# Kernel tuning notes

Measured on AMD Instinct MI355X. Metric: run time of the kernel, lower is better.

## Reference

```python
import jax, jax.numpy as jnp
import numpy as np

B, S, D, H = 4, 2048, 1024, 16
HD = D // H

def setup_inputs() -> dict:
    key = jax.random.key(0)
    ks = jax.random.split(key, 5)
    scale = 1.0 / np.sqrt(D)
    x = jax.random.normal(ks[0], (B, S, D), dtype=jnp.float32)
    w_qkv = jax.random.normal(ks[1], (D, 3 * D), dtype=jnp.float32) * scale
    b_qkv = jax.random.normal(ks[2], (3 * D,), dtype=jnp.float32) * 0.01
    w_proj = jax.random.normal(ks[3], (D, D), dtype=jnp.float32) * scale
    b_proj = jax.random.normal(ks[4], (D,), dtype=jnp.float32) * 0.01
    return {"x": x, "w_qkv": w_qkv, "b_qkv": b_qkv, "w_proj": w_proj, "b_proj": b_proj}

def reference(x, w_qkv, b_qkv, w_proj, b_proj):
    b, s, d = x.shape
    qkv = x @ w_qkv + b_qkv                      # [B,S,3D]
    qkv = qkv.reshape(b, s, 3, H, HD)
    q, k, v = jnp.moveaxis(qkv, 2, 0)            # each [B,S,H,HD]
    q = q.transpose(0, 2, 1, 3)                  # [B,H,S,HD]
    k = k.transpose(0, 2, 1, 3)
    v = v.transpose(0, 2, 1, 3)
    scale = 1.0 / jnp.sqrt(jnp.asarray(HD, dtype=x.dtype))
    scores = jnp.einsum('bhqd,bhkd->bhqk', q, k) * scale
    attn = jax.nn.softmax(scores, axis=-1)
    out = jnp.einsum('bhqk,bhkd->bhqd', attn, v)  # [B,H,S,HD]
    out = out.transpose(0, 2, 1, 3).reshape(b, s, d)
    return out @ w_proj + b_proj
```

## Files before the change

kernel.cpp:

```cpp
#include <hip/hip_runtime.h>

#define B_  4
#define S_  2048
#define D_  1024
#define H_  16
#define HD_ 64
#define M_  (B_*S_)
#define QSCALE 0.1803368801111204f

typedef unsigned short u16;
typedef __bf16 bf16x8 __attribute__((ext_vector_type(8)));
typedef __bf16 bf16x2 __attribute__((ext_vector_type(2)));
typedef float  f32x4  __attribute__((ext_vector_type(4)));
typedef float  f32x16 __attribute__((ext_vector_type(16)));

__device__ __forceinline__ u16 f2bf(float f) {
  unsigned int u = __float_as_uint(f);
  u += 0x7fffu + ((u >> 16) & 1u);
  return (u16)(u >> 16);
}
__device__ __forceinline__ unsigned int packbf2(float lo, float hi) {
#if __has_builtin(__builtin_amdgcn_cvt_pk_bf16_f32)
  union { bf16x2 v; unsigned int u; } c;
  c.v = __builtin_amdgcn_cvt_pk_bf16_f32(lo, hi);
  return c.u;
#else
  return (unsigned int)f2bf(lo) | ((unsigned int)f2bf(hi) << 16);
#endif
}
__device__ __forceinline__ void gld16(const void* g, void* l) {
  __builtin_amdgcn_global_load_lds(
      (const __attribute__((address_space(1))) unsigned int*)g,
      (__attribute__((address_space(3))) unsigned int*)l, 16, 0, 0);
}
#define MFMA32(a,b,c) __builtin_amdgcn_mfma_f32_32x32x16_bf16(a,b,c,0,0,0)
#define MFMA16(a,b,c) __builtin_amdgcn_mfma_f32_16x16x32_bf16(a,b,c,0,0,0)

__global__ void cvt_f32_bf16(const float* __restrict__ in, u16* __restrict__ out, int n4) {
  int i = blockIdx.x * 256 + threadIdx.x;
  if (i < n4) {
    float4 v = ((const float4*)in)[i];
    ((uint2*)out)[i] = make_uint2(packbf2(v.x, v.y), packbf2(v.z, v.w));
  }
}

__global__ void transpose_w(const float* __restrict__ in, u16* __restrict__ out, int R, int C) {
  __shared__ float tile[32][33];
  int c0 = blockIdx.x * 32, r0 = blockIdx.y * 32;
  int tx = threadIdx.x, ty = threadIdx.y;
  #pragma unroll
  for (int i = 0; i < 4; i++)
    tile[ty + i*8][tx] = in[(size_t)(r0 + ty + i*8) * C + c0 + tx];
  __syncthreads();
  #pragma unroll
  for (int i = 0; i < 4; i++)
    out[(size_t)(c0 + ty + i*8) * R + r0 + tx] = f2bf(tile[tx][ty + i*8]);
}

__global__ void transpose_v(const u16* __restrict__ in, u16* __restrict__ out) {
  __shared__ u16 tile[32][33];
  size_t base = (size_t)blockIdx.z * S_ * HD_;
  int c0 = blockIdx.x * 32, r0 = blockIdx.y * 32;
  int tx = threadIdx.x, ty = threadIdx.y;
  #pragma unroll
  for (int i = 0; i < 4; i++)
    tile[ty + i*8][tx] = in[base + (size_t)(r0 + ty + i*8) * HD_ + c0 + tx];
  __syncthreads();
  #pragma unroll
  for (int i = 0; i < 4; i++)
    out[base + (size_t)(c0 + ty + i*8) * S_ + r0 + tx] = tile[tx][ty + i*8];
}

__global__ __launch_bounds__(256) void gemm_qkv(
    const u16* __restrict__ X, const u16* __restrict__ WT,
    const float* __restrict__ bias,
    u16* __restrict__ qb, u16* __restrict__ kb, u16* __restrict__ vb)
{
  __shared__ u16 Al[128 * 40];
  __shared__ u16 Bl[128 * 40];
  const int t = threadIdx.x;
  const int m0 = blockIdx.y * 128;
  const int n0 = blockIdx.x * 128;
  const int wave = t >> 6, lane = t & 63;
  const int wm = (wave >> 1) * 64, wn = (wave & 1) * 64;
  const int lr = lane & 15, quad = lane >> 4;

  f32x4 acc[4][4] = {};
  for (int k0 = 0; k0 < D_; k0 += 32) {
    __syncthreads();
    #pragma unroll
    for (int i = 0; i < 2; i++) {
      int c = t + i * 256;
      int row = c >> 2, ko = (c & 3) * 8;
      *(uint4*)&Al[row * 40 + ko] = *(const uint4*)&X [(size_t)(m0 + row) * D_ + k0 + ko];
      *(uint4*)&Bl[row * 40 + ko] = *(const uint4*)&WT[(size_t)(n0 + row) * D_ + k0 + ko];
    }
    __syncthreads();
    bf16x8 a[4], b[4];
    #pragma unroll
    for (int mt = 0; mt < 4; mt++) a[mt] = *(const bf16x8*)&Al[(wm + mt*16 + lr) * 40 + quad * 8];
    #pragma unroll
    for (int nt = 0; nt < 4; nt++) b[nt] = *(const bf16x8*)&Bl[(wn + nt*16 + lr) * 40 + quad * 8];
    #pragma unroll
    for (int mt = 0; mt < 4; mt++)
      #pragma unroll
      for (int nt = 0; nt < 4; nt++)
        acc[mt][nt] = MFMA16(a[mt], b[nt], acc[mt][nt]);
  }
  #pragma unroll
  for (int mt = 0; mt < 4; mt++)
  #pragma unroll
  for (int nt = 0; nt < 4; nt++)
  #pragma unroll
  for (int r = 0; r < 4; r++) {
    int m = m0 + wm + mt * 16 + quad * 4 + r;
    int n = n0 + wn + nt * 16 + lr;
    float v = acc[mt][nt][r] + bias[n];
    int which = n >> 10;
    int h = (n >> 6) & 15, hd = n & 63;
    int bb = m >> 11, s = m & 2047;
    size_t idx = (((size_t)(bb * H_ + h) * S_) + s) * HD_ + hd;
    if (which == 0)      qb[idx] = f2bf(v * QSCALE);
    else if (which == 1) kb[idx] = f2bf(v);
    else                 vb[idx] = f2bf(v);
  }
}

__global__ __launch_bounds__(256) void gemm_proj(
    const u16* __restrict__ X, const u16* __restrict__ WT,
    const float* __restrict__ bias, float* __restrict__ out)
{
  __shared__ u16 Al[128 * 40];
  __shared__ u16 Bl[128 * 40];
  const int t = threadIdx.x;
  const int m0 = blockIdx.y * 128;
  const int n0 = blockIdx.x * 128;
  const int wave = t >> 6, lane = t & 63;
  const int wm = (wave >> 1) * 64, wn = (wave & 1) * 64;
  const int lr = lane & 15, quad = lane >> 4;

  f32x4 acc[4][4] = {};
  for (int k0 = 0; k0 < D_; k0 += 32) {
    __syncthreads();
    #pragma unroll
    for (int i = 0; i < 2; i++) {
      int c = t + i * 256;
      int row = c >> 2, ko = (c & 3) * 8;
      *(uint4*)&Al[row * 40 + ko] = *(const uint4*)&X [(size_t)(m0 + row) * D_ + k0 + ko];
      *(uint4*)&Bl[row * 40 + ko] = *(const uint4*)&WT[(size_t)(n0 + row) * D_ + k0 + ko];
    }
    __syncthreads();
    bf16x8 a[4], b[4];
    #pragma unroll
    for (int mt = 0; mt < 4; mt++) a[mt] = *(const bf16x8*)&Al[(wm + mt*16 + lr) * 40 + quad * 8];
    #pragma unroll
    for (int nt = 0; nt < 4; nt++) b[nt] = *(const bf16x8*)&Bl[(wn + nt*16 + lr) * 40 + quad * 8];
    #pragma unroll
    for (int mt = 0; mt < 4; mt++)
      #pragma unroll
      for (int nt = 0; nt < 4; nt++)
        acc[mt][nt] = MFMA16(a[mt], b[nt], acc[mt][nt]);
  }
  #pragma unroll
  for (int mt = 0; mt < 4; mt++)
  #pragma unroll
  for (int nt = 0; nt < 4; nt++)
  #pragma unroll
  for (int r = 0; r < 4; r++) {
    int m = m0 + wm + mt * 16 + quad * 4 + r;
    int n = n0 + wn + nt * 16 + lr;
    out[(size_t)m * D_ + n] = acc[mt][nt][r] + bias[n];
  }
}

__global__ __launch_bounds__(128,2) void attn(
    const u16* __restrict__ qb, const u16* __restrict__ kb,
    const u16* __restrict__ vt, u16* __restrict__ ob)
{
  __shared__ u16 Kl[8*512];
  __shared__ u16 Vl[8*512];
  __shared__ float redL[2][64];
  const int t = threadIdx.x, w = t >> 6, l = t & 63, l31 = l & 31, h = l >> 5;
  const int bh = blockIdx.y, b = bh >> 4, hh = bh & 15;
  const int s0 = blockIdx.x * 128 + w * 64;
  const u16* qp = qb + (size_t)bh * S_ * HD_;
  const u16* kp = kb + (size_t)bh * S_ * HD_;
  const u16* vp = vt + (size_t)bh * HD_ * S_;

  bf16x8 qa[2][4];
  #pragma unroll
  for (int g = 0; g < 2; g++)
    #pragma unroll
    for (int kk = 0; kk < 4; kk++)
      qa[g][kk] = *(const bf16x8*)(qp + (size_t)(s0 + g*32 + l31)*HD_ + kk*16 + h*8);

  f32x16 o[2][2] = {};
  float l_[2] = {0.f, 0.f};

  for (int k0 = 0; k0 < S_; k0 += 64) {
    __syncthreads();
    #pragma unroll
    for (int j = 0; j < 4; j++) {
      gld16(kp + (size_t)(k0 + w*32 + l31)*HD_ + j*16 + h*8, (char*)Kl + (w*4+j)*1024);
      gld16(vp + (size_t)(w*32 + l31)*S_ + k0 + j*16 + h*8, (char*)Vl + (w*4+j)*1024);
    }
    __syncthreads();

    f32x16 sf[2][2] = {};
    #pragma unroll
    for (int kk = 0; kk < 4; kk++) {
      bf16x8 ka0 = *(const bf16x8*)(Kl + (0*4+kk)*512 + l*8);
      bf16x8 ka1 = *(const bf16x8*)(Kl + (1*4+kk)*512 + l*8);
      sf[0][0] = MFMA32(ka0, qa[0][kk], sf[0][0]);
      sf[0][1] = MFMA32(ka0, qa[1][kk], sf[0][1]);
      sf[1][0] = MFMA32(ka1, qa[0][kk], sf[1][0]);
      sf[1][1] = MFMA32(ka1, qa[1][kk], sf[1][1]);
    }

    unsigned int pk[2][2][4][2];
    #pragma unroll
    for (int g = 0; g < 2; g++) {
      float sa = 0.f, sb = 0.f, sc = 0.f, sd = 0.f;
      #pragma unroll
      for (int mt = 0; mt < 2; mt++)
        #pragma unroll
        for (int e = 0; e < 4; e++) {
          float p0 = __builtin_amdgcn_exp2f(sf[mt][g][4*e+0]);
          float p1 = __builtin_amdgcn_exp2f(sf[mt][g][4*e+1]);
          float p2 = __builtin_amdgcn_exp2f(sf[mt][g][4*e+2]);
          float p3 = __builtin_amdgcn_exp2f(sf[mt][g][4*e+3]);
          sa += p0; sb += p1; sc += p2; sd += p3;
          pk[mt][g][e][0] = packbf2(p0, p1);
          pk[mt][g][e][1] = packbf2(p2, p3);
        }
      float s = (sa + sb) + (sc + sd);
      s += __shfl_xor(s, 32);
      l_[g] += s;
    }

    #pragma unroll
    for (int kk2 = 0; kk2 < 4; kk2++) {
      const int mt = kk2 >> 1, k1 = kk2 & 1;
      bf16x8 bv0 = *(const bf16x8*)(Vl + (0*4+kk2)*512 + l*8);
      bf16x8 bv1 = *(const bf16x8*)(Vl + (1*4+kk2)*512 + l*8);
      #pragma unroll
      for (int g = 0; g < 2; g++) {
        unsigned int s0_ = h ? pk[mt][g][2*k1][0] : pk[mt][g][2*k1+1][0];
        unsigned int s1_ = h ? pk[mt][g][2*k1][1] : pk[mt][g][2*k1+1][1];
        unsigned int r0 = (unsigned int)__shfl_xor((int)s0_, 32);
        unsigned int r1 = (unsigned int)__shfl_xor((int)s1_, 32);
        union { unsigned int u[4]; bf16x8 v; } pa;
        pa.u[0] = h ? r0 : pk[mt][g][2*k1][0];
        pa.u[1] = h ? r1 : pk[mt][g][2*k1][1];
        pa.u[2] = h ? pk[mt][g][2*k1+1][0] : r0;
        pa.u[3] = h ? pk[mt][g][2*k1+1][1] : r1;
        o[g][0] = MFMA32(pa.v, bv0, o[g][0]);
        o[g][1] = MFMA32(pa.v, bv1, o[g][1]);
      }
    }
  }

  #pragma unroll
  for (int g = 0; g < 2; g++) redL[w][g*32 + l31] = 1.f / l_[g];
  __syncthreads();
  #pragma unroll
  for (int g = 0; g < 2; g++)
    #pragma unroll
    for (int rb = 0; rb < 4; rb++) {
      f32x4 iv4 = *(const f32x4*)&redL[w][g*32 + 8*rb + 4*h];
      #pragma unroll
      for (int c = 0; c < 4; c++) {
        int r = rb*4 + c;
        int row = s0 + g*32 + c + 8*rb + 4*h;
        size_t off = ((size_t)(b*S_ + row)) * D_ + hh*64;
        ob[off + 0*32 + l31] = f2bf(o[g][0][r] * iv4[c]);
        ob[off + 1*32 + l31] = f2bf(o[g][1][r] * iv4[c]);
      }
    }
}

extern "C" void kernel_launch(void* const* d_in, const int* in_sizes, int n_in,
                              void* d_out, int out_size, void* d_ws, size_t ws_size,
                              hipStream_t stream) {
  const float* x      = (const float*)d_in[0];
  const float* w_qkv  = (const float*)d_in[1];
  const float* b_qkv  = (const float*)d_in[2];
  const float* w_proj = (const float*)d_in[3];
  const float* b_proj = (const float*)d_in[4];
  float* out = (float*)d_out;

  char* ws = (char*)d_ws;
  u16* xbf    = (u16*)ws; ws += (size_t)M_ * D_ * 2;
  u16* wqkvT  = (u16*)ws; ws += (size_t)3 * D_ * D_ * 2;
  u16* wprojT = (u16*)ws; ws += (size_t)D_ * D_ * 2;
  u16* qbuf   = (u16*)ws; ws += (size_t)M_ * D_ * 2;
  u16* kbuf   = (u16*)ws; ws += (size_t)M_ * D_ * 2;
  u16* vbuf   = (u16*)ws; ws += (size_t)M_ * D_ * 2;
  u16* vtbuf  = (u16*)ws; ws += (size_t)M_ * D_ * 2;
  u16* aobuf  = (u16*)ws; ws += (size_t)M_ * D_ * 2;

  cvt_f32_bf16<<<(M_ * D_ / 4 + 255) / 256, 256, 0, stream>>>(x, xbf, M_ * D_ / 4);
  transpose_w<<<dim3(3 * D_ / 32, D_ / 32), dim3(32, 8), 0, stream>>>(w_qkv, wqkvT, D_, 3 * D_);
  transpose_w<<<dim3(D_ / 32, D_ / 32), dim3(32, 8), 0, stream>>>(w_proj, wprojT, D_, D_);
  gemm_qkv<<<dim3(3 * D_ / 128, M_ / 128), 256, 0, stream>>>(xbf, wqkvT, b_qkv, qbuf, kbuf, vbuf);
  transpose_v<<<dim3(HD_ / 32, S_ / 32, B_ * H_), dim3(32, 8), 0, stream>>>(vbuf, vtbuf);
  attn<<<dim3(S_ / 128, B_ * H_), 128, 0, stream>>>(qbuf, kbuf, vtbuf, aobuf);
  gemm_proj<<<dim3(D_ / 128, M_ / 128), 256, 0, stream>>>(aobuf, wprojT, b_proj, out);
}
```

Baseline: 324.2 us.

## Pre-tile operands into MFMA fragment layout and double-buffer LDS with async loads

Producer kernels now write X, the weights, Q/K, V and the attention output directly in a tiled layout that matches the MFMA fragment order. The GEMM and attention kernels can then use contiguous global_load_lds copies into double-buffered shared memory, prefetching the next tile while computing the current one. The separate V transpose kernel and its buffer are removed because the QKV GEMM epilogue writes V already transposed. The producers now do scattered 2-byte stores, and the larger LDS footprint may limit occupancy.

```diff
diff --git a/kernel.cpp b/kernel.cpp
--- a/kernel.cpp
+++ b/kernel.cpp
@@ -36,11 +36,27 @@
 #define MFMA32(a,b,c) __builtin_amdgcn_mfma_f32_32x32x16_bf16(a,b,c,0,0,0)
 #define MFMA16(a,b,c) __builtin_amdgcn_mfma_f32_16x16x32_bf16(a,b,c,0,0,0)
 
+__device__ __forceinline__ size_t off16e(int r, int k) {
+  return ((size_t)((r >> 7) * 32 + (k >> 5))) * 4096
+       + (size_t)((r >> 4) & 7) * 512
+       + (size_t)(((k >> 3) & 3) * 16 + (r & 15)) * 8 + (k & 7);
+}
+__device__ __forceinline__ size_t offA32(int bh, int s, int hd) {
+  return ((size_t)(bh * 32 + (s >> 6)) * 8 + ((s >> 5) & 1) * 4 + (hd >> 4)) * 512
+       + (size_t)(((hd >> 3) & 1) * 32 + (s & 31)) * 8 + (hd & 7);
+}
+__device__ __forceinline__ size_t offVT(int bh, int s, int hd) {
+  return ((size_t)(bh * 32 + (s >> 6)) * 8 + (hd >> 5) * 4 + ((s >> 4) & 3)) * 512
+       + (size_t)(((s >> 3) & 1) * 32 + (hd & 31)) * 8 + (s & 7);
+}
+
 __global__ void cvt_f32_bf16(const float* __restrict__ in, u16* __restrict__ out, int n4) {
   int i = blockIdx.x * 256 + threadIdx.x;
   if (i < n4) {
     float4 v = ((const float4*)in)[i];
-    ((uint2*)out)[i] = make_uint2(packbf2(v.x, v.y), packbf2(v.z, v.w));
+    int m = i >> 8;
+    int k = (i & 255) * 4;
+    *(uint2*)&out[off16e(m, k)] = make_uint2(packbf2(v.x, v.y), packbf2(v.z, v.w));
   }
 }
 
@@ -54,122 +70,124 @@
   __syncthreads();
   #pragma unroll
   for (int i = 0; i < 4; i++)
-    out[(size_t)(c0 + ty + i*8) * R + r0 + tx] = f2bf(tile[tx][ty + i*8]);
-}
-
-__global__ void transpose_v(const u16* __restrict__ in, u16* __restrict__ out) {
-  __shared__ u16 tile[32][33];
-  size_t base = (size_t)blockIdx.z * S_ * HD_;
-  int c0 = blockIdx.x * 32, r0 = blockIdx.y * 32;
-  int tx = threadIdx.x, ty = threadIdx.y;
-  #pragma unroll
-  for (int i = 0; i < 4; i++)
-    tile[ty + i*8][tx] = in[base + (size_t)(r0 + ty + i*8) * HD_ + c0 + tx];
-  __syncthreads();
-  #pragma unroll
-  for (int i = 0; i < 4; i++)
-    out[base + (size_t)(c0 + ty + i*8) * S_ + r0 + tx] = tile[tx][ty + i*8];
-}
-
-__global__ __launch_bounds__(256) void gemm_qkv(
+    out[off16e(c0 + ty + i*8, r0 + tx)] = f2bf(tile[tx][ty + i*8]);
+}
+
+__global__ __launch_bounds__(256,2) void gemm_qkv(
     const u16* __restrict__ X, const u16* __restrict__ WT,
     const float* __restrict__ bias,
     u16* __restrict__ qb, u16* __restrict__ kb, u16* __restrict__ vb)
 {
-  __shared__ u16 Al[128 * 40];
-  __shared__ u16 Bl[128 * 40];
-  const int t = threadIdx.x;
-  const int m0 = blockIdx.y * 128;
-  const int n0 = blockIdx.x * 128;
-  const int wave = t >> 6, lane = t & 63;
-  const int wm = (wave >> 1) * 64, wn = (wave & 1) * 64;
-  const int lr = lane & 15, quad = lane >> 4;
-
+  __shared__ u16 As[2*8*512];
+  __shared__ u16 Bs[2*8*512];
+  const int t = threadIdx.x, w = t >> 6, l = t & 63;
+  const int m0 = blockIdx.y * 128, n0 = blockIdx.x * 128;
+  const u16* Ab = X  + (size_t)(m0 >> 7) * 32 * 4096;
+  const u16* Bb = WT + (size_t)(n0 >> 7) * 32 * 4096;
+
+  #pragma unroll
+  for (int f2 = 0; f2 < 2; f2++) {
+    gld16(Ab + (w*2+f2)*512 + l*8, (char*)As + (w*2+f2)*1024);
+    gld16(Bb + (w*2+f2)*512 + l*8, (char*)Bs + (w*2+f2)*1024);
+  }
   f32x4 acc[4][4] = {};
-  for (int k0 = 0; k0 < D_; k0 += 32) {
+  const int af = (w >> 1) * 4, bf = (w & 1) * 4;
+  for (int it = 0; it < 32; it++) {
     __syncthreads();
-    #pragma unroll
-    for (int i = 0; i < 2; i++) {
-      int c = t + i * 256;
-      int row = c >> 2, ko = (c & 3) * 8;
-      *(uint4*)&Al[row * 40 + ko] = *(const uint4*)&X [(size_t)(m0 + row) * D_ + k0 + ko];
-      *(uint4*)&Bl[row * 40 + ko] = *(const uint4*)&WT[(size_t)(n0 + row) * D_ + k0 + ko];
-    }
-    __syncthreads();
+    const int cur = (it & 1) * 4096;
+    if (it < 31) {
+      const int nb = ((it + 1) & 1) * 8;
+      const size_t gs = (size_t)(it + 1) * 4096;
+      #pragma unroll
+      for (int f2 = 0; f2 < 2; f2++) {
+        gld16(Ab + gs + (w*2+f2)*512 + l*8, (char*)As + (nb + w*2+f2)*1024);
+        gld16(Bb + gs + (w*2+f2)*512 + l*8, (char*)Bs + (nb + w*2+f2)*1024);
+      }
+    }
     bf16x8 a[4], b[4];
     #pragma unroll
-    for (int mt = 0; mt < 4; mt++) a[mt] = *(const bf16x8*)&Al[(wm + mt*16 + lr) * 40 + quad * 8];
-    #pragma unroll
-    for (int nt = 0; nt < 4; nt++) b[nt] = *(const bf16x8*)&Bl[(wn + nt*16 + lr) * 40 + quad * 8];
+    for (int mt = 0; mt < 4; mt++) a[mt] = *(const bf16x8*)(As + cur + (af+mt)*512 + l*8);
+    #pragma unroll
+    for (int nt = 0; nt < 4; nt++) b[nt] = *(const bf16x8*)(Bs + cur + (bf+nt)*512 + l*8);
     #pragma unroll
     for (int mt = 0; mt < 4; mt++)
       #pragma unroll
       for (int nt = 0; nt < 4; nt++)
         acc[mt][nt] = MFMA16(a[mt], b[nt], acc[mt][nt]);
   }
+  const int wm = (w >> 1) * 64, wn = (w & 1) * 64, lr = l & 15, quad = l >> 4;
   #pragma unroll
   for (int mt = 0; mt < 4; mt++)
   #pragma unroll
-  for (int nt = 0; nt < 4; nt++)
-  #pragma unroll
-  for (int r = 0; r < 4; r++) {
-    int m = m0 + wm + mt * 16 + quad * 4 + r;
+  for (int nt = 0; nt < 4; nt++) {
     int n = n0 + wn + nt * 16 + lr;
-    float v = acc[mt][nt][r] + bias[n];
-    int which = n >> 10;
-    int h = (n >> 6) & 15, hd = n & 63;
-    int bb = m >> 11, s = m & 2047;
-    size_t idx = (((size_t)(bb * H_ + h) * S_) + s) * HD_ + hd;
-    if (which == 0)      qb[idx] = f2bf(v * QSCALE);
-    else if (which == 1) kb[idx] = f2bf(v);
-    else                 vb[idx] = f2bf(v);
-  }
-}
-
-__global__ __launch_bounds__(256) void gemm_proj(
+    float bia = bias[n];
+    int which = n >> 10, hh = (n >> 6) & 15, hd = n & 63;
+    #pragma unroll
+    for (int r = 0; r < 4; r++) {
+      int m = m0 + wm + mt * 16 + quad * 4 + r;
+      float v = acc[mt][nt][r] + bia;
+      int bb = m >> 11, s = m & 2047, bh = bb * 16 + hh;
+      if (which == 0)      qb[offA32(bh, s, hd)] = f2bf(v * QSCALE);
+      else if (which == 1) kb[offA32(bh, s, hd)] = f2bf(v);
+      else                 vb[offVT(bh, s, hd)] = f2bf(v);
+    }
+  }
+}
+
+__global__ __launch_bounds__(256,2) void gemm_proj(
     const u16* __restrict__ X, const u16* __restrict__ WT,
     const float* __restrict__ bias, float* __restrict__ out)
 {
-  __shared__ u16 Al[128 * 40];
-  __shared__ u16 Bl[128 * 40];
-  const int t = threadIdx.x;
-  const int m0 = blockIdx.y * 128;
-  const int n0 = blockIdx.x * 128;
-  const int wave = t >> 6, lane = t & 63;
-  const int wm = (wave >> 1) * 64, wn = (wave & 1) * 64;
-  const int lr = lane & 15, quad = lane >> 4;
-
+  __shared__ u16 As[2*8*512];
+  __shared__ u16 Bs[2*8*512];
+  const int t = threadIdx.x, w = t >> 6, l = t & 63;
+  const int m0 = blockIdx.y * 128, n0 = blockIdx.x * 128;
+  const u16* Ab = X  + (size_t)(m0 >> 7) * 32 * 4096;
+  const u16* Bb = WT + (size_t)(n0 >> 7) * 32 * 4096;
+
+  #pragma unroll
+  for (int f2 = 0; f2 < 2; f2++) {
+    gld16(Ab + (w*2+f2)*512 + l*8, (char*)As + (w*2+f2)*1024);
+    gld16(Bb + (w*2+f2)*512 + l*8, (char*)Bs + (w*2+f2)*1024);
+  }
   f32x4 acc[4][4] = {};
-  for (int k0 = 0; k0 < D_; k0 += 32) {
+  const int af = (w >> 1) * 4, bf = (w & 1) * 4;
+  for (int it = 0; it < 32; it++) {
     __syncthreads();
-    #pragma unroll
-    for (int i = 0; i < 2; i++) {
-      int c = t + i * 256;
-      int row = c >> 2, ko = (c & 3) * 8;
-      *(uint4*)&Al[row * 40 + ko] = *(const uint4*)&X [(size_t)(m0 + row) * D_ + k0 + ko];
-      *(uint4*)&Bl[row * 40 + ko] = *(const uint4*)&WT[(size_t)(n0 + row) * D_ + k0 + ko];
-    }
-    __syncthreads();
+    const int cur = (it & 1) * 4096;
+    if (it < 31) {
+      const int nb = ((it + 1) & 1) * 8;
+      const size_t gs = (size_t)(it + 1) * 4096;
+      #pragma unroll
+      for (int f2 = 0; f2 < 2; f2++) {
+        gld16(Ab + gs + (w*2+f2)*512 + l*8, (char*)As + (nb + w*2+f2)*1024);
+        gld16(Bb + gs + (w*2+f2)*512 + l*8, (char*)Bs + (nb + w*2+f2)*1024);
+      }
+    }
     bf16x8 a[4], b[4];
     #pragma unroll
-    for (int mt = 0; mt < 4; mt++) a[mt] = *(const bf16x8*)&Al[(wm + mt*16 + lr) * 40 + quad * 8];
-    #pragma unroll
-    for (int nt = 0; nt < 4; nt++) b[nt] = *(const bf16x8*)&Bl[(wn + nt*16 + lr) * 40 + quad * 8];
+    for (int mt = 0; mt < 4; mt++) a[mt] = *(const bf16x8*)(As + cur + (af+mt)*512 + l*8);
+    #pragma unroll
+    for (int nt = 0; nt < 4; nt++) b[nt] = *(const bf16x8*)(Bs + cur + (bf+nt)*512 + l*8);
     #pragma unroll
     for (int mt = 0; mt < 4; mt++)
       #pragma unroll
       for (int nt = 0; nt < 4; nt++)
         acc[mt][nt] = MFMA16(a[mt], b[nt], acc[mt][nt]);
   }
+  const int wm = (w >> 1) * 64, wn = (w & 1) * 64, lr = l & 15, quad = l >> 4;
   #pragma unroll
   for (int mt = 0; mt < 4; mt++)
   #pragma unroll
-  for (int nt = 0; nt < 4; nt++)
-  #pragma unroll
-  for (int r = 0; r < 4; r++) {
-    int m = m0 + wm + mt * 16 + quad * 4 + r;
+  for (int nt = 0; nt < 4; nt++) {
     int n = n0 + wn + nt * 16 + lr;
-    out[(size_t)m * D_ + n] = acc[mt][nt][r] + bias[n];
+    float bia = bias[n];
+    #pragma unroll
+    for (int r = 0; r < 4; r++) {
+      int m = m0 + wm + mt * 16 + quad * 4 + r;
+      out[(size_t)m * D_ + n] = acc[mt][nt][r] + bia;
+    }
   }
 }
 
@@ -177,40 +195,51 @@
     const u16* __restrict__ qb, const u16* __restrict__ kb,
     const u16* __restrict__ vt, u16* __restrict__ ob)
 {
-  __shared__ u16 Kl[8*512];
-  __shared__ u16 Vl[8*512];
+  __shared__ u16 Kl[2*8*512];
+  __shared__ u16 Vl[2*8*512];
   __shared__ float redL[2][64];
   const int t = threadIdx.x, w = t >> 6, l = t & 63, l31 = l & 31, h = l >> 5;
   const int bh = blockIdx.y, b = bh >> 4, hh = bh & 15;
-  const int s0 = blockIdx.x * 128 + w * 64;
-  const u16* qp = qb + (size_t)bh * S_ * HD_;
-  const u16* kp = kb + (size_t)bh * S_ * HD_;
-  const u16* vp = vt + (size_t)bh * HD_ * S_;
+  const int qt = blockIdx.x;
+  const int s0 = qt * 128 + w * 64;
+  const u16* qp = qb + (size_t)bh * 131072;
+  const u16* kp = kb + (size_t)bh * 131072;
+  const u16* vp = vt + (size_t)bh * 131072;
 
   bf16x8 qa[2][4];
   #pragma unroll
   for (int g = 0; g < 2; g++)
     #pragma unroll
     for (int kk = 0; kk < 4; kk++)
-      qa[g][kk] = *(const bf16x8*)(qp + (size_t)(s0 + g*32 + l31)*HD_ + kk*16 + h*8);
+      qa[g][kk] = *(const bf16x8*)(qp + ((size_t)(qt*2 + w) * 8 + g*4 + kk) * 512 + l*8);
 
   f32x16 o[2][2] = {};
   float l_[2] = {0.f, 0.f};
 
-  for (int k0 = 0; k0 < S_; k0 += 64) {
+  #pragma unroll
+  for (int j = 0; j < 4; j++) {
+    gld16(kp + (size_t)(w*4 + j) * 512 + l*8, (char*)Kl + (w*4 + j)*1024);
+    gld16(vp + (size_t)(w*4 + j) * 512 + l*8, (char*)Vl + (w*4 + j)*1024);
+  }
+
+  for (int kt = 0; kt < 32; kt++) {
     __syncthreads();
-    #pragma unroll
-    for (int j = 0; j < 4; j++) {
-      gld16(kp + (size_t)(k0 + w*32 + l31)*HD_ + j*16 + h*8, (char*)Kl + (w*4+j)*1024);
-      gld16(vp + (size_t)(w*32 + l31)*S_ + k0 + j*16 + h*8, (char*)Vl + (w*4+j)*1024);
-    }
-    __syncthreads();
+    const int cur = (kt & 1) * 4096;
+    if (kt < 31) {
+      const int nb = ((kt + 1) & 1) * 8;
+      const size_t gs = (size_t)(kt + 1) * 4096;
+      #pragma unroll
+      for (int j = 0; j < 4; j++) {
+        gld16(kp + gs + (w*4 + j)*512 + l*8, (char*)Kl + (nb + w*4 + j)*1024);
+        gld16(vp + gs + (w*4 + j)*512 + l*8, (char*)Vl + (nb + w*4 + j)*1024);
+      }
+    }
 
     f32x16 sf[2][2] = {};
     #pragma unroll
     for (int kk = 0; kk < 4; kk++) {
-      bf16x8 ka0 = *(const bf16x8*)(Kl + (0*4+kk)*512 + l*8);
-      bf16x8 ka1 = *(const bf16x8*)(Kl + (1*4+kk)*512 + l*8);
+      bf16x8 ka0 = *(const bf16x8*)(Kl + cur + (0*4 + kk)*512 + l*8);
+      bf16x8 ka1 = *(const bf16x8*)(Kl + cur + (1*4 + kk)*512 + l*8);
       sf[0][0] = MFMA32(ka0, qa[0][kk], sf[0][0]);
       sf[0][1] = MFMA32(ka0, qa[1][kk], sf[0][1]);
       sf[1][0] = MFMA32(ka1, qa[0][kk], sf[1][0]);
@@ -241,8 +270,8 @@
     #pragma unroll
     for (int kk2 = 0; kk2 < 4; kk2++) {
       const int mt = kk2 >> 1, k1 = kk2 & 1;
-      bf16x8 bv0 = *(const bf16x8*)(Vl + (0*4+kk2)*512 + l*8);
-      bf16x8 bv1 = *(const bf16x8*)(Vl + (1*4+kk2)*512 + l*8);
+      bf16x8 bv0 = *(const bf16x8*)(Vl + cur + (0*4 + kk2)*512 + l*8);
+      bf16x8 bv1 = *(const bf16x8*)(Vl + cur + (1*4 + kk2)*512 + l*8);
       #pragma unroll
       for (int g = 0; g < 2; g++) {
         unsigned int s0_ = h ? pk[mt][g][2*k1][0] : pk[mt][g][2*k1+1][0];
@@ -272,9 +301,10 @@
       for (int c = 0; c < 4; c++) {
         int r = rb*4 + c;
         int row = s0 + g*32 + c + 8*rb + 4*h;
-        size_t off = ((size_t)(b*S_ + row)) * D_ + hh*64;
-        ob[off + 0*32 + l31] = f2bf(o[g][0][r] * iv4[c]);
-        ob[off + 1*32 + l31] = f2bf(o[g][1][r] * iv4[c]);
+        int m = b * S_ + row;
+        int d0 = hh*64 + l31, d1 = hh*64 + 32 + l31;
+        ob[off16e(m, d0)] = f2bf(o[g][0][r] * iv4[c]);
+        ob[off16e(m, d1)] = f2bf(o[g][1][r] * iv4[c]);
       }
     }
 }
@@ -295,15 +325,13 @@
   u16* wprojT = (u16*)ws; ws += (size_t)D_ * D_ * 2;
   u16* qbuf   = (u16*)ws; ws += (size_t)M_ * D_ * 2;
   u16* kbuf   = (u16*)ws; ws += (size_t)M_ * D_ * 2;
-  u16* vbuf   = (u16*)ws; ws += (size_t)M_ * D_ * 2;
   u16* vtbuf  = (u16*)ws; ws += (size_t)M_ * D_ * 2;
   u16* aobuf  = (u16*)ws; ws += (size_t)M_ * D_ * 2;
 
   cvt_f32_bf16<<<(M_ * D_ / 4 + 255) / 256, 256, 0, stream>>>(x, xbf, M_ * D_ / 4);
   transpose_w<<<dim3(3 * D_ / 32, D_ / 32), dim3(32, 8), 0, stream>>>(w_qkv, wqkvT, D_, 3 * D_);
   transpose_w<<<dim3(D_ / 32, D_ / 32), dim3(32, 8), 0, stream>>>(w_proj, wprojT, D_, D_);
-  gemm_qkv<<<dim3(3 * D_ / 128, M_ / 128), 256, 0, stream>>>(xbf, wqkvT, b_qkv, qbuf, kbuf, vbuf);
-  transpose_v<<<dim3(HD_ / 32, S_ / 32, B_ * H_), dim3(32, 8), 0, stream>>>(vbuf, vtbuf);
+  gemm_qkv<<<dim3(3 * D_ / 128, M_ / 128), 256, 0, stream>>>(xbf, wqkvT, b_qkv, qbuf, kbuf, vtbuf);
   attn<<<dim3(S_ / 128, B_ * H_), 128, 0, stream>>>(qbuf, kbuf, vtbuf, aobuf);
   gemm_proj<<<dim3(D_ / 128, M_ / 128), 256, 0, stream>>>(aobuf, wprojT, b_proj, out);
 }
```

New measurement: 317.2 us. -2.2%, faster.
